# Kernel tuning notes

Measured on AMD Instinct MI355X. Metric: run time of the kernel, lower is better.

The kernel has to match this reference:

```python
import jax, jax.numpy as jnp
import numpy as np

PC_RANGE = (-51.2, -51.2, -5.0, 51.2, 51.2, 3.0)
E, CAMS, LVLS = 256, 6, 4
LVL_HW = [(64, 176), (32, 88), (16, 44), (8, 22)]


def setup_inputs() -> dict:
    key = jax.random.key(0)
    ks = jax.random.split(key, 16)
    B, N = 2, 6400
    inp = {
        'instance_feature': jax.random.normal(ks[0], (B, N, E), jnp.float32),
        'anchor': jax.random.normal(ks[1], (B, N, 11), jnp.float32),
        'projection': jax.random.uniform(ks[2], (B, CAMS, 4, 4), jnp.float32),
    }
    for i, (H, W) in enumerate(LVL_HW):
        inp[f'feat{i}'] = jax.random.normal(ks[3 + i], (B, CAMS, E, H, W), jnp.float32)
    # learned params (random, not the zero-init of the module, to exercise the math)
    inp['attn_w'] = jax.random.normal(ks[8], (CAMS * LVLS, E), jnp.float32) * 0.02
    inp['attn_b'] = jax.random.normal(ks[9], (CAMS * LVLS,), jnp.float32) * 0.02
    inp['vp_w'] = jax.random.normal(ks[10], (E, E), jnp.float32) * (1.0 / np.sqrt(E))
    inp['vp_b'] = jnp.zeros((E,), jnp.float32)
    inp['op_w'] = jax.random.normal(ks[11], (E, E), jnp.float32) * (1.0 / np.sqrt(E))
    inp['op_b'] = jnp.zeros((E,), jnp.float32)
    return inp


def _bilinear_sample(feat, x, y):
    """feat: [BN, C, H, W]; x, y: [BN, N] pixel coords.
    Bilinear, zeros padding, align_corners=True (pixel coords == uv directly).
    Returns [BN, N, C]."""
    BN, C, H, W = feat.shape
    x0 = jnp.floor(x); y0 = jnp.floor(y)
    wx1 = x - x0; wx0 = 1.0 - wx1
    wy1 = y - y0; wy0 = 1.0 - wy1
    feat_flat = feat.reshape(BN, C, H * W)
    b = jnp.arange(BN)[:, None]

    def corner(xi, yi, w):
        valid = (xi >= 0) & (xi <= W - 1) & (yi >= 0) & (yi <= H - 1)
        xi_c = jnp.clip(xi, 0, W - 1).astype(jnp.int32)
        yi_c = jnp.clip(yi, 0, H - 1).astype(jnp.int32)
        idx = yi_c * W + xi_c                      # [BN, N]
        v = feat_flat[b, :, idx]                   # [BN, N, C]
        return v * (w * valid.astype(w.dtype))[..., None]

    return (corner(x0, y0, wx0 * wy0) + corner(x0 + 1, y0, wx1 * wy0)
            + corner(x0, y0 + 1, wx0 * wy1) + corner(x0 + 1, y0 + 1, wx1 * wy1))


def reference(instance_feature, anchor, projection, feat0, feat1, feat2, feat3,
              attn_w, attn_b, vp_w, vp_b, op_w, op_b):
    B, N, _ = instance_feature.shape
    feats = [feat0, feat1, feat2, feat3]
    # attention weights over cams x levels (softmax over levels, dim=-1)
    attn = (instance_feature @ attn_w.T + attn_b).reshape(B, N, CAMS, LVLS)
    attn = jax.nn.softmax(attn, axis=-1)
    # anchor center -> world coords
    xyz = jax.nn.sigmoid(anchor[..., :3])
    pr = jnp.asarray(PC_RANGE, dtype=anchor.dtype)
    xyz_world = xyz * (pr[3:6] - pr[0:3]) + pr[0:3]
    xyz_h = jnp.concatenate([xyz_world, jnp.ones((B, N, 1), anchor.dtype)], axis=-1)
    xyz_cam = jnp.einsum('bcij,bnj->bcni', projection, xyz_h)   # [B,CAMS,N,4]
    depth = jnp.maximum(xyz_cam[..., 2:3], 1e-4)
    uv = xyz_cam[..., :2] / depth                               # [B,CAMS,N,2] pixel coords
    BN = B * CAMS
    x = uv[..., 0].reshape(BN, N)
    y = uv[..., 1].reshape(BN, N)
    sampled = []
    for feat in feats:
        H, W = feat.shape[-2], feat.shape[-1]
        s = _bilinear_sample(feat.reshape(BN, E, H, W), x, y)   # [BN,N,E]
        sampled.append(s.reshape(B, CAMS, N, E))
    S = jnp.stack(sampled, axis=0)                              # [L,B,CAMS,N,E]
    out = jnp.einsum('lbcne,bncl->bne', S, attn)
    out = out @ vp_w.T + vp_b
    out = (out + instance_feature) @ op_w.T + op_b
    return out
```

## Files before the change

kernel.cpp:

```cpp
#include <hip/hip_runtime.h>
#include <hip/hip_fp16.h>
#include <math.h>

#define B_ 2
#define N_ 6400
#define E_ 256
#define C_ 6
#define L_ 4
#define SL2_ 128

__device__ __host__ constexpr int HWH[4] = {64, 32, 16, 8};
__device__ __host__ constexpr int HWW[4] = {176, 88, 44, 22};
__device__ __host__ constexpr int LOFF[4] = {0, 11264, 14080, 14784};
#define HWT 14960

typedef __attribute__((ext_vector_type(8))) _Float16 half8;
typedef __attribute__((ext_vector_type(4))) float floatx4;

__global__ __launch_bounds__(256) void prep_kernel(
    const float* __restrict__ inst, const float* __restrict__ anchor,
    const float* __restrict__ proj, const float* __restrict__ attn_w,
    const float* __restrict__ attn_b,
    uint4* __restrict__ meta_w, int4* __restrict__ meta_b)
{
    __shared__ float AWT[256 * 24];
    __shared__ float ts[256 * 33];

    const int tid = threadIdx.x;

    for (int idx = tid; idx < 24 * 256; idx += 256) {
        int j = idx >> 8, k = idx & 255;
        AWT[k * 24 + j] = attn_w[idx];
    }
    __syncthreads();

    const int pt0 = blockIdx.x * 256;

    float acc[24];
#pragma unroll
    for (int j = 0; j < 24; j++) acc[j] = attn_b[j];

    for (int k0 = 0; k0 < 256; k0 += 32) {
#pragma unroll
        for (int r = 0; r < 32; r++) {
            int lin = r * 256 + tid;
            int p = lin >> 5, kk = lin & 31;
            ts[p * 33 + kk] = inst[(size_t)(pt0 + p) * 256 + k0 + kk];
        }
        __syncthreads();
#pragma unroll
        for (int kk = 0; kk < 32; kk++) {
            float v = ts[tid * 33 + kk];
            const float* aw = &AWT[(k0 + kk) * 24];
#pragma unroll
            for (int j = 0; j < 24; j++) acc[j] += v * aw[j];
        }
        __syncthreads();
    }

    const int pt = pt0 + tid;
    const int b = pt / N_;
    const int n = pt - b * N_;

    float attn[24];
#pragma unroll
    for (int c = 0; c < C_; c++) {
        float m = fmaxf(fmaxf(acc[c * 4], acc[c * 4 + 1]),
                        fmaxf(acc[c * 4 + 2], acc[c * 4 + 3]));
        float s = 0.f;
#pragma unroll
        for (int l = 0; l < L_; l++) {
            float e = expf(acc[c * 4 + l] - m);
            attn[c * 4 + l] = e;
            s += e;
        }
        float r = 1.f / s;
#pragma unroll
        for (int l = 0; l < L_; l++) attn[c * 4 + l] *= r;
    }

    float ax = anchor[(size_t)pt * 11 + 0];
    float ay = anchor[(size_t)pt * 11 + 1];
    float az = anchor[(size_t)pt * 11 + 2];
    float wxp = (1.f / (1.f + expf(-ax))) * 102.4f - 51.2f;
    float wyp = (1.f / (1.f + expf(-ay))) * 102.4f - 51.2f;
    float wzp = (1.f / (1.f + expf(-az))) * 8.f - 5.f;

#pragma unroll
    for (int c = 0; c < C_; c++) {
        const float* P = &proj[(size_t)(b * C_ + c) * 16];
        float cx = P[0] * wxp + P[1] * wyp + P[2] * wzp + P[3];
        float cy = P[4] * wxp + P[5] * wyp + P[6] * wzp + P[7];
        float cz = P[8] * wxp + P[9] * wyp + P[10] * wzp + P[11];
        float d = fmaxf(cz, 1e-4f);
        float u = cx / d, v = cy / d;

        float x0f = floorf(u), y0f = floorf(v);
        float fx1 = u - x0f, fy1 = v - y0f;
        float fx0 = 1.f - fx1, fy0 = 1.f - fy1;

        float4 wl[4]; int bsx[4];
#pragma unroll
        for (int l = 0; l < L_; l++) {
            const int W = HWW[l], H = HWH[l];
            float ax0, ax1; int bx;
            int ix = (int)fminf(fmaxf(x0f, -2.f), (float)W);
            if (ix <= -2 || ix >= W)      { ax0 = 0.f;  ax1 = 0.f;  bx = 0; }
            else if (ix == -1)            { ax0 = fx1;  ax1 = 0.f;  bx = 0; }
            else if (ix == W - 1)         { ax0 = 0.f;  ax1 = fx0;  bx = W - 2; }
            else                          { ax0 = fx0;  ax1 = fx1;  bx = ix; }
            float ay0, ay1; int by;
            int iy = (int)fminf(fmaxf(y0f, -2.f), (float)H);
            if (iy <= -2 || iy >= H)      { ay0 = 0.f;  ay1 = 0.f;  by = 0; }
            else if (iy == -1)            { ay0 = fy1;  ay1 = 0.f;  by = 0; }
            else if (iy == H - 1)         { ay0 = 0.f;  ay1 = fy0;  by = H - 2; }
            else                          { ay0 = fy0;  ay1 = fy1;  by = iy; }

            float a = attn[c * 4 + l];
            wl[l] = make_float4(a * ay0 * ax0, a * ay0 * ax1,
                                a * ay1 * ax0, a * ay1 * ax1);
            bsx[l] = by * W + bx;
        }
        size_t mi = (size_t)(b * C_ + c) * N_ + n;
        union { uint4 u; __half2 h[4]; } q0, q1;
        q0.h[0] = __floats2half2_rn(wl[0].x, wl[0].y);
        q0.h[1] = __floats2half2_rn(wl[0].z, wl[0].w);
        q0.h[2] = __floats2half2_rn(wl[1].x, wl[1].y);
        q0.h[3] = __floats2half2_rn(wl[1].z, wl[1].w);
        q1.h[0] = __floats2half2_rn(wl[2].x, wl[2].y);
        q1.h[1] = __floats2half2_rn(wl[2].z, wl[2].w);
        q1.h[2] = __floats2half2_rn(wl[3].x, wl[3].y);
        q1.h[3] = __floats2half2_rn(wl[3].z, wl[3].w);
        meta_w[mi * 2 + 0] = q0.u;
        meta_w[mi * 2 + 1] = q1.u;
        meta_b[mi] = make_int4(bsx[0], bsx[1], bsx[2], bsx[3]);
    }
}

template<bool PART>
__global__ __launch_bounds__(1024) void gather_t(
    const float* __restrict__ f0, const float* __restrict__ f1,
    const float* __restrict__ f2, const float* __restrict__ f3,
    const uint4* __restrict__ meta_w, const int4* __restrict__ meta_b,
    __half2* __restrict__ part2, float* __restrict__ agg)
{
    __shared__ __half2 lds2[HWT];

    const int tid = threadIdx.x;
    const int bid = blockIdx.x;
    const int slice = bid & 127;
    const int c = (bid >> 7) % C_;
    const int b = bid / (128 * C_);
    const int e0 = slice * 2;
    const int bc = b * C_ + c;

    const float* fs[4] = {f0, f1, f2, f3};

#pragma unroll
    for (int l = 0; l < L_; l++) {
        const int HW = HWH[l] * HWW[l];
        const float* s0 = fs[l] + (size_t)(bc * E_ + e0) * HW;
        const float* s1 = s0 + HW;
        const int quarter = HW >> 2;
        for (int q = tid; q < quarter; q += 1024) {
            int p = q * 4;
            float4 v0 = *(const float4*)(s0 + p);
            float4 v1 = *(const float4*)(s1 + p);
            union { uint4 u; __half2 h[4]; } pk;
            pk.h[0] = __floats2half2_rn(v0.x, v1.x);
            pk.h[1] = __floats2half2_rn(v0.y, v1.y);
            pk.h[2] = __floats2half2_rn(v0.z, v1.z);
            pk.h[3] = __floats2half2_rn(v0.w, v1.w);
            *(uint4*)&lds2[LOFF[l] + p] = pk.u;
        }
    }
    __syncthreads();

    const size_t mbase = (size_t)bc * N_;
    const uint4* mwp = meta_w + mbase * 2;
    const int4* mbp = meta_b + mbase;
    __half2* pout = part2 + ((size_t)bc * SL2_ + slice) * N_;
    float* aggb = agg + (size_t)b * N_ * E_ + e0;

    int n = tid;
    uint4 m0, m1; int4 px;
    uint4 o0, o1; int4 ox;
    {
        m0 = mwp[(size_t)n * 2];
        m1 = mwp[(size_t)n * 2 + 1];
        px = mbp[n];
    }
    if (n + 1024 < N_) {
        o0 = mwp[(size_t)(n + 1024) * 2];
        o1 = mwp[(size_t)(n + 1024) * 2 + 1];
        ox = mbp[n + 1024];
    }

    while (n < N_) {
        const int n2 = n + 2048;
        uint4 t0, t1; int4 tx;
        if (n2 < N_) {
            t0 = mwp[(size_t)n2 * 2];
            t1 = mwp[(size_t)n2 * 2 + 1];
            tx = mbp[n2];
        }

        union { uint4 u; __half2 h[4]; } a0u, a1u;
        a0u.u = m0; a1u.u = m1;
        const int pxs[4] = {px.x, px.y, px.z, px.w};

        __half2 accA = __float2half2_rn(0.f);
        __half2 accB = __float2half2_rn(0.f);
#pragma unroll
        for (int l = 0; l < L_; l++) {
            const int W = HWW[l];
            const int base = LOFF[l] + pxs[l];
            const __half2 wp0 = (l < 2) ? a0u.h[(l & 1) * 2]     : a1u.h[(l & 1) * 2];
            const __half2 wp1 = (l < 2) ? a0u.h[(l & 1) * 2 + 1] : a1u.h[(l & 1) * 2 + 1];
            const __half2 w00 = __half2half2(__low2half(wp0));
            const __half2 w01 = __half2half2(__high2half(wp0));
            const __half2 w10 = __half2half2(__low2half(wp1));
            const __half2 w11 = __half2half2(__high2half(wp1));
            accA = __hfma2(w00, lds2[base],         accA);
            accA = __hfma2(w01, lds2[base + 1],     accA);
            accB = __hfma2(w10, lds2[base + W],     accB);
            accB = __hfma2(w11, lds2[base + W + 1], accB);
        }
        const __half2 acc = __hadd2(accA, accB);

        if (PART) {
            pout[n] = acc;
        } else {
            float2 af = __half22float2(acc);
            if (af.x != 0.f || af.y != 0.f) {
                float* dst = aggb + (size_t)n * E_;
                atomicAdd(dst + 0, af.x);
                atomicAdd(dst + 1, af.y);
            }
        }

        n += 1024;
        m0 = o0; m1 = o1; px = ox;
        o0 = t0; o1 = t1; ox = tx;
    }
}

#define SAS2 264
#define WSS2 72
#define KC 64

__global__ __launch_bounds__(1024, 4) void gemm_mfma(
    const float* __restrict__ inst,
    const float* __restrict__ vp_w, const float* __restrict__ vp_b,
    const float* __restrict__ op_w, const float* __restrict__ op_b,
    const __half2* __restrict__ part2, float* __restrict__ out)
{
    __shared__ _Float16 sA[128 * SAS2];
    __shared__ _Float16 wS[256 * WSS2];

    const int tid = threadIdx.x;
    const int wave = tid >> 6;
    const int lane = tid & 63;
    const int mt = wave & 7;
    const int nh = wave >> 3;
    const int q = lane >> 4;
    const int col = lane & 15;

    const int p0 = blockIdx.x * 128;
    const int b = p0 / N_;
    const int nbase = p0 - b * N_;

    {
        const int p = tid & 127, sg = tid >> 7;
        const int n = nbase + p;
        for (int s = sg; s < SL2_; s += 8) {
            float a0 = 0.f, a1 = 0.f;
#pragma unroll
            for (int c = 0; c < C_; c++) {
                float2 f = __half22float2(
                    part2[((size_t)(b * C_ + c) * SL2_ + s) * N_ + n]);
                a0 += f.x; a1 += f.y;
            }
            sA[p * SAS2 + s * 2 + 0] = (_Float16)a0;
            sA[p * SAS2 + s * 2 + 1] = (_Float16)a1;
        }
    }

    floatx4 acc[8];
#pragma unroll
    for (int nt = 0; nt < 8; nt++) acc[nt] = (floatx4)(0.f);

    for (int kc = 0; kc < 256 / KC; kc++) {
        __syncthreads();
        {
            const int row = tid >> 2, qt = tid & 3;
            const float* src = vp_w + (size_t)row * 256 + kc * KC + qt * 16;
            _Float16* dst = &wS[row * WSS2 + qt * 16];
#pragma unroll
            for (int i = 0; i < 2; i++) {
                float4 v = *(const float4*)(src + i * 8);
                float4 u = *(const float4*)(src + i * 8 + 4);
                half8 h = {(_Float16)v.x, (_Float16)v.y, (_Float16)v.z, (_Float16)v.w,
                           (_Float16)u.x, (_Float16)u.y, (_Float16)u.z, (_Float16)u.w};
                *(half8*)(dst + i * 8) = h;
            }
        }
        __syncthreads();
#pragma unroll
        for (int ks = 0; ks < KC / 32; ks++) {
            half8 a = *(half8*)&sA[(mt * 16 + col) * SAS2 + kc * KC + ks * 32 + q * 8];
#pragma unroll
            for (int nt = 0; nt < 8; nt++) {
                half8 bf = *(half8*)&wS[(nh * 128 + nt * 16 + col) * WSS2 + ks * 32 + q * 8];
                acc[nt] = __builtin_amdgcn_mfma_f32_16x16x32_f16(a, bf, acc[nt], 0, 0, 0);
            }
        }
    }

    __syncthreads();
#pragma unroll
    for (int nt = 0; nt < 8; nt++) {
        const int e = nh * 128 + nt * 16 + col;
        const float bv = vp_b[e];
#pragma unroll
        for (int r = 0; r < 4; r++) {
            const int p = mt * 16 + q * 4 + r;
            float t = acc[nt][r] + bv + inst[(size_t)(p0 + p) * E_ + e];
            sA[p * SAS2 + e] = (_Float16)t;
        }
        acc[nt] = (floatx4)(0.f);
    }

    for (int kc = 0; kc < 256 / KC; kc++) {
        __syncthreads();
        {
            const int row = tid >> 2, qt = tid & 3;
            const float* src = op_w + (size_t)row * 256 + kc * KC + qt * 16;
            _Float16* dst = &wS[row * WSS2 + qt * 16];
#pragma unroll
            for (int i = 0; i < 2; i++) {
                float4 v = *(const float4*)(src + i * 8);
                float4 u = *(const float4*)(src + i * 8 + 4);
                half8 h = {(_Float16)v.x, (_Float16)v.y, (_Float16)v.z, (_Float16)v.w,
                           (_Float16)u.x, (_Float16)u.y, (_Float16)u.z, (_Float16)u.w};
                *(half8*)(dst + i * 8) = h;
            }
        }
        __syncthreads();
#pragma unroll
        for (int ks = 0; ks < KC / 32; ks++) {
            half8 a = *(half8*)&sA[(mt * 16 + col) * SAS2 + kc * KC + ks * 32 + q * 8];
#pragma unroll
            for (int nt = 0; nt < 8; nt++) {
                half8 bf = *(half8*)&wS[(nh * 128 + nt * 16 + col) * WSS2 + ks * 32 + q * 8];
                acc[nt] = __builtin_amdgcn_mfma_f32_16x16x32_f16(a, bf, acc[nt], 0, 0, 0);
            }
        }
    }

#pragma unroll
    for (int nt = 0; nt < 8; nt++) {
        const int e = nh * 128 + nt * 16 + col;
        const float ob = op_b[e];
#pragma unroll
        for (int r = 0; r < 4; r++) {
            const int p = mt * 16 + q * 4 + r;
            out[(size_t)(p0 + p) * E_ + e] = acc[nt][r] + ob;
        }
    }
}

#define PT 32
#define SAS 264
#define WSS 36

__global__ __launch_bounds__(256) void gemm_valu(
    const float* __restrict__ inst,
    const float* __restrict__ vp_w, const float* __restrict__ vp_b,
    const float* __restrict__ op_w, const float* __restrict__ op_b,
    float* __restrict__ io)
{
    __shared__ __align__(16) float sA[PT * SAS];
    __shared__ __align__(16) float wS[256 * WSS];

    const int tid = threadIdx.x;
    const int eg = tid & 31;
    const int pg = tid >> 5;
    const int p0 = blockIdx.x * PT;

#pragma unroll
    for (int r = 0; r < PT; r++)
        sA[r * SAS + tid] = io[(size_t)(p0 + r) * E_ + tid];
    __syncthreads();

    float acc[4][8];
#pragma unroll
    for (int j = 0; j < 4; j++)
#pragma unroll
        for (int i = 0; i < 8; i++) acc[j][i] = 0.f;

    for (int k0 = 0; k0 < 256; k0 += 32) {
        __syncthreads();
#pragma unroll
        for (int r = 0; r < 32; r++) {
            int lin = r * 256 + tid;
            int e = lin >> 5, kk = lin & 31;
            wS[e * WSS + kk] = vp_w[(size_t)e * 256 + k0 + kk];
        }
        __syncthreads();
#pragma unroll
        for (int kk = 0; kk < 32; kk += 4) {
            float4 wv4[8], av4[4];
#pragma unroll
            for (int i = 0; i < 8; i++)
                wv4[i] = *(const float4*)&wS[(eg + 32 * i) * WSS + kk];
#pragma unroll
            for (int j = 0; j < 4; j++)
                av4[j] = *(const float4*)&sA[(pg * 4 + j) * SAS + k0 + kk];
#pragma unroll
            for (int j = 0; j < 4; j++)
#pragma unroll
                for (int i = 0; i < 8; i++)
                    acc[j][i] += av4[j].x * wv4[i].x + av4[j].y * wv4[i].y
                               + av4[j].z * wv4[i].z + av4[j].w * wv4[i].w;
        }
    }

    __syncthreads();
#pragma unroll
    for (int j = 0; j < 4; j++) {
        int p = pg * 4 + j;
#pragma unroll
        for (int i = 0; i < 8; i++) {
            int e = eg + 32 * i;
            float t = acc[j][i] + vp_b[e] + inst[(size_t)(p0 + p) * E_ + e];
            sA[p * SAS + e] = t;
            acc[j][i] = 0.f;
        }
    }

    for (int k0 = 0; k0 < 256; k0 += 32) {
        __syncthreads();
#pragma unroll
        for (int r = 0; r < 32; r++) {
            int lin = r * 256 + tid;
            int e = lin >> 5, kk = lin & 31;
            wS[e * WSS + kk] = op_w[(size_t)e * 256 + k0 + kk];
        }
        __syncthreads();
#pragma unroll
        for (int kk = 0; kk < 32; kk += 4) {
            float4 wv4[8], av4[4];
#pragma unroll
            for (int i = 0; i < 8; i++)
                wv4[i] = *(const float4*)&wS[(eg + 32 * i) * WSS + kk];
#pragma unroll
            for (int j = 0; j < 4; j++)
                av4[j] = *(const float4*)&sA[(pg * 4 + j) * SAS + k0 + kk];
#pragma unroll
            for (int j = 0; j < 4; j++)
#pragma unroll
                for (int i = 0; i < 8; i++)
                    acc[j][i] += av4[j].x * wv4[i].x + av4[j].y * wv4[i].y
                               + av4[j].z * wv4[i].z + av4[j].w * wv4[i].w;
        }
    }

#pragma unroll
    for (int j = 0; j < 4; j++) {
        int p = pg * 4 + j;
#pragma unroll
        for (int i = 0; i < 8; i++) {
            int e = eg + 32 * i;
            io[(size_t)(p0 + p) * E_ + e] = acc[j][i] + op_b[e];
        }
    }
}

extern "C" void kernel_launch(void* const* d_in, const int* in_sizes, int n_in,
                              void* d_out, int out_size, void* d_ws, size_t ws_size,
                              hipStream_t stream)
{
    const float* inst   = (const float*)d_in[0];
    const float* anchor = (const float*)d_in[1];
    const float* proj   = (const float*)d_in[2];
    const float* f0     = (const float*)d_in[3];
    const float* f1     = (const float*)d_in[4];
    const float* f2     = (const float*)d_in[5];
    const float* f3     = (const float*)d_in[6];
    const float* attn_w = (const float*)d_in[7];
    const float* attn_b = (const float*)d_in[8];
    const float* vp_w   = (const float*)d_in[9];
    const float* vp_b   = (const float*)d_in[10];
    const float* op_w   = (const float*)d_in[11];
    const float* op_b   = (const float*)d_in[12];
    float* out = (float*)d_out;

    const size_t NPT = (size_t)B_ * C_ * N_;
    uint4* meta_w = (uint4*)d_ws;
    int4* meta_b = (int4*)((char*)d_ws + NPT * 32);
    __half2* part2 = (__half2*)((char*)d_ws + NPT * 48);
    const size_t part2_bytes = (size_t)B_ * C_ * SL2_ * N_ * sizeof(__half2);
    const size_t need = NPT * 48 + part2_bytes;

    prep_kernel<<<(B_ * N_) / 256, 256, 0, stream>>>(
        inst, anchor, proj, attn_w, attn_b, meta_w, meta_b);

    if (ws_size >= need) {
        gather_t<true><<<B_ * C_ * SL2_, 1024, 0, stream>>>(
            f0, f1, f2, f3, meta_w, meta_b, part2, out);
        gemm_mfma<<<(B_ * N_) / 128, 1024, 0, stream>>>(
            inst, vp_w, vp_b, op_w, op_b, part2, out);
    } else {
        hipMemsetAsync(d_out, 0, (size_t)out_size * sizeof(float), stream);
        gather_t<false><<<B_ * C_ * SL2_, 1024, 0, stream>>>(
            f0, f1, f2, f3, meta_w, meta_b, part2, out);
        gemm_valu<<<(B_ * N_) / PT, 256, 0, stream>>>(
            inst, vp_w, vp_b, op_w, op_b, out);
    }
}
```

Before: 342.7 us.

## Accumulate three cameras per gather block to shrink partial-sum buffer

```diff
diff --git a/kernel.cpp b/kernel.cpp
--- a/kernel.cpp
+++ b/kernel.cpp
@@ -8,6 +8,7 @@
 #define C_ 6
 #define L_ 4
 #define SL2_ 128
+#define CH_ 2
 
 __device__ __host__ constexpr int HWH[4] = {64, 32, 16, 8};
 __device__ __host__ constexpr int HWW[4] = {176, 88, 44, 22};
@@ -137,12 +138,115 @@
     }
 }
 
-template<bool PART>
-__global__ __launch_bounds__(1024) void gather_t(
+__global__ __launch_bounds__(1024) void gather3(
     const float* __restrict__ f0, const float* __restrict__ f1,
     const float* __restrict__ f2, const float* __restrict__ f3,
     const uint4* __restrict__ meta_w, const int4* __restrict__ meta_b,
-    __half2* __restrict__ part2, float* __restrict__ agg)
+    __half2* __restrict__ part2)
+{
+    __shared__ __half2 lds2[HWT];
+
+    const int tid = threadIdx.x;
+    const int bid = blockIdx.x;
+    const int slice = bid & 127;
+    const int chalf = (bid >> 7) & 1;
+    const int b = bid >> 8;
+    const int e0 = slice * 2;
+
+    const float* fs[4] = {f0, f1, f2, f3};
+
+    __half2 acc[7];
+#pragma unroll
+    for (int k = 0; k < 7; k++) acc[k] = __float2half2_rn(0.f);
+
+    for (int cc = 0; cc < 3; cc++) {
+        const int c = chalf * 3 + cc;
+        const int bc = b * C_ + c;
+
+        if (cc) __syncthreads();
+
+#pragma unroll
+        for (int l = 0; l < L_; l++) {
+            const int HW = HWH[l] * HWW[l];
+            const float* s0 = fs[l] + (size_t)(bc * E_ + e0) * HW;
+            const float* s1 = s0 + HW;
+            const int quarter = HW >> 2;
+            for (int q = tid; q < quarter; q += 1024) {
+                int p = q * 4;
+                float4 v0 = *(const float4*)(s0 + p);
+                float4 v1 = *(const float4*)(s1 + p);
+                union { uint4 u; __half2 h[4]; } pk;
+                pk.h[0] = __floats2half2_rn(v0.x, v1.x);
+                pk.h[1] = __floats2half2_rn(v0.y, v1.y);
+                pk.h[2] = __floats2half2_rn(v0.z, v1.z);
+                pk.h[3] = __floats2half2_rn(v0.w, v1.w);
+                *(uint4*)&lds2[LOFF[l] + p] = pk.u;
+            }
+        }
+        __syncthreads();
+
+        const uint4* mwp = meta_w + (size_t)bc * N_ * 2;
+        const int4* mbp = meta_b + (size_t)bc * N_;
+
+        uint4 m0 = mwp[(size_t)tid * 2];
+        uint4 m1 = mwp[(size_t)tid * 2 + 1];
+        int4 px = mbp[tid];
+
+#pragma unroll
+        for (int k = 0; k < 7; k++) {
+            uint4 q0, q1; int4 qx;
+            if (k < 6) {
+                const int nn = tid + (k + 1) * 1024;
+                if (nn < N_) {
+                    q0 = mwp[(size_t)nn * 2];
+                    q1 = mwp[(size_t)nn * 2 + 1];
+                    qx = mbp[nn];
+                }
+            }
+
+            const int n = tid + k * 1024;
+            if (n < N_) {
+                union { uint4 u; __half2 h[4]; } a0u, a1u;
+                a0u.u = m0; a1u.u = m1;
+                const int pxs[4] = {px.x, px.y, px.z, px.w};
+
+                __half2 accA = __float2half2_rn(0.f);
+                __half2 accB = __float2half2_rn(0.f);
+#pragma unroll
+                for (int l = 0; l < L_; l++) {
+                    const int W = HWW[l];
+                    const int base = LOFF[l] + pxs[l];
+                    const __half2 wp0 = (l < 2) ? a0u.h[(l & 1) * 2]     : a1u.h[(l & 1) * 2];
+                    const __half2 wp1 = (l < 2) ? a0u.h[(l & 1) * 2 + 1] : a1u.h[(l & 1) * 2 + 1];
+                    const __half2 w00 = __half2half2(__low2half(wp0));
+                    const __half2 w01 = __half2half2(__high2half(wp0));
+                    const __half2 w10 = __half2half2(__low2half(wp1));
+                    const __half2 w11 = __half2half2(__high2half(wp1));
+                    accA = __hfma2(w00, lds2[base],         accA);
+                    accA = __hfma2(w01, lds2[base + 1],     accA);
+                    accB = __hfma2(w10, lds2[base + W],     accB);
+                    accB = __hfma2(w11, lds2[base + W + 1], accB);
+                }
+                acc[k] = __hadd2(acc[k], __hadd2(accA, accB));
+            }
+
+            if (k < 6) { m0 = q0; m1 = q1; px = qx; }
+        }
+    }
+
+    __half2* pout = part2 + ((size_t)(b * CH_ + chalf) * SL2_ + slice) * N_;
+#pragma unroll
+    for (int k = 0; k < 7; k++) {
+        const int n = tid + k * 1024;
+        if (n < N_) pout[n] = acc[k];
+    }
+}
+
+__global__ __launch_bounds__(1024) void gather_atomic(
+    const float* __restrict__ f0, const float* __restrict__ f1,
+    const float* __restrict__ f2, const float* __restrict__ f3,
+    const uint4* __restrict__ meta_w, const int4* __restrict__ meta_b,
+    float* __restrict__ agg)
 {
     __shared__ __half2 lds2[HWT];
 
@@ -179,31 +283,12 @@
     const size_t mbase = (size_t)bc * N_;
     const uint4* mwp = meta_w + mbase * 2;
     const int4* mbp = meta_b + mbase;
-    __half2* pout = part2 + ((size_t)bc * SL2_ + slice) * N_;
     float* aggb = agg + (size_t)b * N_ * E_ + e0;
 
-    int n = tid;
-    uint4 m0, m1; int4 px;
-    uint4 o0, o1; int4 ox;
-    {
-        m0 = mwp[(size_t)n * 2];
-        m1 = mwp[(size_t)n * 2 + 1];
-        px = mbp[n];
-    }
-    if (n + 1024 < N_) {
-        o0 = mwp[(size_t)(n + 1024) * 2];
-        o1 = mwp[(size_t)(n + 1024) * 2 + 1];
-        ox = mbp[n + 1024];
-    }
-
-    while (n < N_) {
-        const int n2 = n + 2048;
-        uint4 t0, t1; int4 tx;
-        if (n2 < N_) {
-            t0 = mwp[(size_t)n2 * 2];
-            t1 = mwp[(size_t)n2 * 2 + 1];
-            tx = mbp[n2];
-        }
+    for (int n = tid; n < N_; n += 1024) {
+        uint4 m0 = mwp[(size_t)n * 2];
+        uint4 m1 = mwp[(size_t)n * 2 + 1];
+        int4 px = mbp[n];
 
         union { uint4 u; __half2 h[4]; } a0u, a1u;
         a0u.u = m0; a1u.u = m1;
@@ -226,22 +311,12 @@
             accB = __hfma2(w10, lds2[base + W],     accB);
             accB = __hfma2(w11, lds2[base + W + 1], accB);
         }
-        const __half2 acc = __hadd2(accA, accB);
-
-        if (PART) {
-            pout[n] = acc;
-        } else {
-            float2 af = __half22float2(acc);
-            if (af.x != 0.f || af.y != 0.f) {
-                float* dst = aggb + (size_t)n * E_;
-                atomicAdd(dst + 0, af.x);
-                atomicAdd(dst + 1, af.y);
-            }
-        }
-
-        n += 1024;
-        m0 = o0; m1 = o1; px = ox;
-        o0 = t0; o1 = t1; ox = tx;
+        float2 af = __half22float2(__hadd2(accA, accB));
+        if (af.x != 0.f || af.y != 0.f) {
+            float* dst = aggb + (size_t)n * E_;
+            atomicAdd(dst + 0, af.x);
+            atomicAdd(dst + 1, af.y);
+        }
     }
 }
 
@@ -274,15 +349,12 @@
         const int p = tid & 127, sg = tid >> 7;
         const int n = nbase + p;
         for (int s = sg; s < SL2_; s += 8) {
-            float a0 = 0.f, a1 = 0.f;
-#pragma unroll
-            for (int c = 0; c < C_; c++) {
-                float2 f = __half22float2(
-                    part2[((size_t)(b * C_ + c) * SL2_ + s) * N_ + n]);
-                a0 += f.x; a1 += f.y;
-            }
-            sA[p * SAS2 + s * 2 + 0] = (_Float16)a0;
-            sA[p * SAS2 + s * 2 + 1] = (_Float16)a1;
+            float2 fa = __half22float2(
+                part2[((size_t)(b * CH_ + 0) * SL2_ + s) * N_ + n]);
+            float2 fb = __half22float2(
+                part2[((size_t)(b * CH_ + 1) * SL2_ + s) * N_ + n]);
+            sA[p * SAS2 + s * 2 + 0] = (_Float16)(fa.x + fb.x);
+            sA[p * SAS2 + s * 2 + 1] = (_Float16)(fa.y + fb.y);
         }
     }
 
@@ -500,21 +572,21 @@
     uint4* meta_w = (uint4*)d_ws;
     int4* meta_b = (int4*)((char*)d_ws + NPT * 32);
     __half2* part2 = (__half2*)((char*)d_ws + NPT * 48);
-    const size_t part2_bytes = (size_t)B_ * C_ * SL2_ * N_ * sizeof(__half2);
+    const size_t part2_bytes = (size_t)B_ * CH_ * SL2_ * N_ * sizeof(__half2);
     const size_t need = NPT * 48 + part2_bytes;
 
     prep_kernel<<<(B_ * N_) / 256, 256, 0, stream>>>(
         inst, anchor, proj, attn_w, attn_b, meta_w, meta_b);
 
     if (ws_size >= need) {
-        gather_t<true><<<B_ * C_ * SL2_, 1024, 0, stream>>>(
-            f0, f1, f2, f3, meta_w, meta_b, part2, out);
+        gather3<<<B_ * CH_ * SL2_, 1024, 0, stream>>>(
+            f0, f1, f2, f3, meta_w, meta_b, part2);
         gemm_mfma<<<(B_ * N_) / 128, 1024, 0, stream>>>(
             inst, vp_w, vp_b, op_w, op_b, part2, out);
     } else {
         hipMemsetAsync(d_out, 0, (size_t)out_size * sizeof(float), stream);
-        gather_t<false><<<B_ * C_ * SL2_, 1024, 0, stream>>>(
-            f0, f1, f2, f3, meta_w, meta_b, part2, out);
+        gather_atomic<<<B_ * C_ * SL2_, 1024, 0, stream>>>(
+            f0, f1, f2, f3, meta_w, meta_b, out);
         gemm_valu<<<(B_ * N_) / PT, 256, 0, stream>>>(
             inst, vp_w, vp_b, op_w, op_b, out);
     }
```

Result: slower. 469.4 us (+37.0%).
